# Kernel optimization log

Measured on AMD Instinct MI355X. Metric: run time of the kernel, lower is better.

## Reference

```python
import jax, jax.numpy as jnp
import numpy as np

T = 8192  # context/question length (input_shape[2])
D = 128   # feature dim (input_shape[3])


def setup_inputs() -> dict:
    key = jax.random.key(0)
    k1, k2 = jax.random.split(key)
    x = jax.random.normal(k1, (2, 1, T, D), dtype=jnp.float32)
    kernel = jax.random.normal(k2, (3 * D,), dtype=jnp.float32)
    return {"x": x, "kernel": kernel}


def reference(x, kernel):
    context = x[0, 0]   # (T, D)
    question = x[1, 0]  # (T, D)
    w_c, w_q, w_m = kernel[:D], kernel[D:2 * D], kernel[2 * D:]

    # Additive similarity: S[i,j] = c_i.w_c + q_j.w_q + (c_i*q_j).w_m
    # Avoids materializing the (T, T, 3D) tiled/concatenated tensor.
    S = (context @ w_c)[:, None] + (question @ w_q)[None, :] \
        + (context * w_m) @ question.T  # (T, T)

    A = jax.nn.softmax(S, axis=-1)  # row-wise softmax, as tf.nn.softmax on 2D

    # C2Q attention: U_A[i] = sum_j A[i,j] * q_j
    U_A = A @ question  # (T, D)

    # Q2C attention: b = row-max of A, h = sum_i b_i * c_i, tiled over rows
    b = jnp.max(A, axis=1)          # (T,)
    h = b @ context                 # (D,)
    H_A = jnp.broadcast_to(h, (T, D))

    # megamerge: [c, U_A, c*U_A, c*H_A]
    G = jnp.concatenate([context, U_A, context * U_A, context * H_A], axis=-1)
    return G  # (T, 4D)
```

## Files before the change

kernel.cpp:

```cpp
#include <hip/hip_runtime.h>
#include <hip/hip_bf16.h>

#define T 8192
#define D 128
#define NSPLIT 8
#define JLEN (T / NSPLIT)
#define BN 64
#define NITER (JLEN / BN)
#define BM 128
#define LOG2E 1.44269504088896f

typedef _Float16 half4_t __attribute__((ext_vector_type(4)));
typedef _Float16 half8_t __attribute__((ext_vector_type(8)));
typedef float floatx4 __attribute__((ext_vector_type(4)));

__global__ void prep_kernel(const float* __restrict__ x, const float* __restrict__ kern,
                            _Float16* __restrict__ q16, _Float16* __restrict__ qT16,
                            _Float16* __restrict__ cm16, float* __restrict__ qq2) {
    const float* context  = x;
    const float* question = x + (size_t)T * D;
    const float* wq = kern + D;
    const float* wm = kern + 2 * D;
    __shared__ __align__(16) _Float16 tile[32][136];
    int j0 = blockIdx.x * 32;
    int t = threadIdx.x;
    int c4 = t & 31;
    int rsub = t >> 5;
    float4 wqv = ((const float4*)wq)[c4];
    float4 wmv = ((const float4*)wm)[c4];
    for (int p = 0; p < 4; ++p) {
        int row = p * 8 + rsub;
        float4 q = ((const float4*)(question + (size_t)(j0 + row) * D))[c4];
        float4 c = ((const float4*)(context  + (size_t)(j0 + row) * D))[c4];
        half4_t qh;
        qh[0] = (_Float16)q.x; qh[1] = (_Float16)q.y; qh[2] = (_Float16)q.z; qh[3] = (_Float16)q.w;
        *(half4_t*)(q16 + (size_t)(j0 + row) * D + c4 * 4) = qh;
        *(half4_t*)&tile[row][c4 * 4] = qh;
        half4_t ch;
        ch[0] = (_Float16)(c.x * wmv.x * LOG2E); ch[1] = (_Float16)(c.y * wmv.y * LOG2E);
        ch[2] = (_Float16)(c.z * wmv.z * LOG2E); ch[3] = (_Float16)(c.w * wmv.w * LOG2E);
        *(half4_t*)(cm16 + (size_t)(j0 + row) * D + c4 * 4) = ch;
        float s = q.x * wqv.x + q.y * wqv.y + q.z * wqv.z + q.w * wqv.w;
        for (int dx = 1; dx <= 16; dx <<= 1) s += __shfl_xor(s, dx);
        if (c4 == 0) qq2[j0 + row] = s * LOG2E;
    }
    __syncthreads();
    for (int p = 0; p < 2; ++p) {
        int chunk = t + p * 256;
        int d = chunk >> 2, jo = (chunk & 3) * 8;
        half8_t v;
        for (int s2 = 0; s2 < 8; ++s2) v[s2] = tile[jo + s2][d];
        *(half8_t*)(qT16 + (size_t)d * T + j0 + jo) = v;
    }
}

__global__ __launch_bounds__(256, 2)
void flash_kernel(const _Float16* __restrict__ q16, const _Float16* __restrict__ qT16,
                  const _Float16* __restrict__ cm16, const float* __restrict__ qq2,
                  _Float16* __restrict__ Opart, float* __restrict__ mpart,
                  float* __restrict__ lpart) {
    __shared__ __align__(16) _Float16 Kt[2][64][144];
    __shared__ __align__(16) _Float16 Vt[2][128][72];
    __shared__ __align__(16) float qqs[JLEN];

    int bx = blockIdx.x;
    int rb = bx >> 3;
    int sp = bx & 7;
    int tid = threadIdx.x;
    int wave = tid >> 6;
    int lane = tid & 63;
    int quad = lane >> 4;
    int l15 = lane & 15;
    int rbase = rb * BM + wave * 32;

    ((float4*)qqs)[tid] = ((const float4*)(qq2 + (size_t)sp * JLEN))[tid];

    half8_t qfrag[2][4];
    for (int mt = 0; mt < 2; ++mt)
        for (int ks = 0; ks < 4; ++ks)
            qfrag[mt][ks] = *(const half8_t*)(cm16 + (size_t)(rbase + mt * 16 + l15) * D
                                              + ks * 32 + quad * 8);

    floatx4 acc[2][8];
    for (int mt = 0; mt < 2; ++mt)
        for (int nt = 0; nt < 8; ++nt)
            for (int r = 0; r < 4; ++r) acc[mt][nt][r] = 0.f;
    float m_run[2] = {-INFINITY, -INFINITY};
    float l_run[2] = {0.f, 0.f};

    half8_t kreg[4];
    half4_t vlo[4], vhi[4];

    {
        int j0 = sp * JLEN;
        for (int k = 0; k < 4; ++k) {
            int idx = tid + k * 256;
            kreg[k] = *(const half8_t*)(q16 + (size_t)(j0 + (idx >> 4)) * D + (idx & 15) * 8);
            int dr = idx >> 3, c8 = idx & 7;
            int base = j0 + (c8 >> 2) * 32 + (c8 & 3) * 4;
            vlo[k] = *(const half4_t*)(qT16 + (size_t)dr * T + base);
            vhi[k] = *(const half4_t*)(qT16 + (size_t)dr * T + base + 16);
        }
    }

    for (int it = 0; it < NITER; ++it) {
        int b = it & 1;
        for (int k = 0; k < 4; ++k) {
            int idx = tid + k * 256;
            *(half8_t*)&Kt[b][idx >> 4][(idx & 15) * 8] = kreg[k];
            half8_t v;
            v[0] = vlo[k][0]; v[1] = vlo[k][1]; v[2] = vlo[k][2]; v[3] = vlo[k][3];
            v[4] = vhi[k][0]; v[5] = vhi[k][1]; v[6] = vhi[k][2]; v[7] = vhi[k][3];
            *(half8_t*)&Vt[b][idx >> 3][(idx & 7) * 8] = v;
        }
        __syncthreads();

        if (it + 1 < NITER) {
            int j0n = sp * JLEN + (it + 1) * BN;
            for (int k = 0; k < 4; ++k) {
                int idx = tid + k * 256;
                kreg[k] = *(const half8_t*)(q16 + (size_t)(j0n + (idx >> 4)) * D + (idx & 15) * 8);
                int dr = idx >> 3, c8 = idx & 7;
                int base = j0n + (c8 >> 2) * 32 + (c8 & 3) * 4;
                vlo[k] = *(const half4_t*)(qT16 + (size_t)dr * T + base);
                vhi[k] = *(const half4_t*)(qT16 + (size_t)dr * T + base + 16);
            }
        }

        floatx4 St[2][4];
        for (int mt = 0; mt < 2; ++mt)
            for (int jt = 0; jt < 4; ++jt)
                for (int r = 0; r < 4; ++r) St[mt][jt][r] = 0.f;
        for (int ks = 0; ks < 4; ++ks)
            for (int jt = 0; jt < 4; ++jt) {
                half8_t a = *(const half8_t*)&Kt[b][jt * 16 + l15][ks * 32 + quad * 8];
                St[0][jt] = __builtin_amdgcn_mfma_f32_16x16x32_f16(a, qfrag[0][ks], St[0][jt], 0, 0, 0);
                St[1][jt] = __builtin_amdgcn_mfma_f32_16x16x32_f16(a, qfrag[1][ks], St[1][jt], 0, 0, 0);
            }

        float4 bias[4];
        for (int jt = 0; jt < 4; ++jt)
            bias[jt] = *(const float4*)&qqs[it * 64 + jt * 16 + quad * 4];
        for (int mt = 0; mt < 2; ++mt) {
            St[mt][0][0] += bias[0].x; St[mt][0][1] += bias[0].y; St[mt][0][2] += bias[0].z; St[mt][0][3] += bias[0].w;
            St[mt][1][0] += bias[1].x; St[mt][1][1] += bias[1].y; St[mt][1][2] += bias[1].z; St[mt][1][3] += bias[1].w;
            St[mt][2][0] += bias[2].x; St[mt][2][1] += bias[2].y; St[mt][2][2] += bias[2].z; St[mt][2][3] += bias[2].w;
            St[mt][3][0] += bias[3].x; St[mt][3][1] += bias[3].y; St[mt][3][2] += bias[3].z; St[mt][3][3] += bias[3].w;
        }

        half4_t apv[2][4];
        float alpha[2];
        for (int mt = 0; mt < 2; ++mt) {
            float mx = St[mt][0][0];
            for (int jt = 0; jt < 4; ++jt)
                for (int r = 0; r < 4; ++r) mx = fmaxf(mx, St[mt][jt][r]);
            mx = fmaxf(mx, __shfl_xor(mx, 16));
            mx = fmaxf(mx, __shfl_xor(mx, 32));
            float mnew = fmaxf(m_run[mt], mx);
            alpha[mt] = __builtin_amdgcn_exp2f(m_run[mt] - mnew);
            m_run[mt] = mnew;
            float ps = 0.f;
            for (int jt = 0; jt < 4; ++jt) {
                float p0 = __builtin_amdgcn_exp2f(St[mt][jt][0] - mnew);
                float p1 = __builtin_amdgcn_exp2f(St[mt][jt][1] - mnew);
                float p2 = __builtin_amdgcn_exp2f(St[mt][jt][2] - mnew);
                float p3 = __builtin_amdgcn_exp2f(St[mt][jt][3] - mnew);
                ps += (p0 + p1) + (p2 + p3);
                apv[mt][jt][0] = (_Float16)p0;
                apv[mt][jt][1] = (_Float16)p1;
                apv[mt][jt][2] = (_Float16)p2;
                apv[mt][jt][3] = (_Float16)p3;
            }
            ps += __shfl_xor(ps, 16);
            ps += __shfl_xor(ps, 32);
            l_run[mt] = l_run[mt] * alpha[mt] + ps;
        }
        for (int mt = 0; mt < 2; ++mt) {
            float aT[4];
            for (int r = 0; r < 4; ++r)
                aT[r] = __shfl(alpha[mt], quad * 4 + r);
            for (int nt = 0; nt < 8; ++nt)
                for (int r = 0; r < 4; ++r) acc[mt][nt][r] *= aT[r];
        }

        for (int pr = 0; pr < 2; ++pr) {
            half8_t bb[8];
            for (int nt = 0; nt < 8; ++nt)
                bb[nt] = *(const half8_t*)&Vt[b][nt * 16 + l15][pr * 32 + quad * 8];
            for (int h = 0; h < 2; ++h) {
                int jt = pr * 2 + h;
                for (int nt = 0; nt < 8; ++nt) {
                    half4_t bv;
                    bv[0] = bb[nt][h * 4 + 0]; bv[1] = bb[nt][h * 4 + 1];
                    bv[2] = bb[nt][h * 4 + 2]; bv[3] = bb[nt][h * 4 + 3];
                    acc[0][nt] = __builtin_amdgcn_mfma_f32_16x16x16f16(apv[0][jt], bv, acc[0][nt], 0, 0, 0);
                    acc[1][nt] = __builtin_amdgcn_mfma_f32_16x16x16f16(apv[1][jt], bv, acc[1][nt], 0, 0, 0);
                }
            }
        }
    }

    for (int mt = 0; mt < 2; ++mt) {
        if (quad == 0) {
            int iq = rbase + mt * 16 + l15;
            mpart[(size_t)sp * T + iq] = m_run[mt];
            lpart[(size_t)sp * T + iq] = l_run[mt];
        }
        int i = rbase + mt * 16 + quad * 4;
        for (int nt = 0; nt < 8; ++nt)
            for (int r = 0; r < 4; ++r)
                Opart[((size_t)sp * T + (i + r)) * D + nt * 16 + l15] = (_Float16)acc[mt][nt][r];
    }
}

__global__ void merge_kernel(const _Float16* __restrict__ Opart, const float* __restrict__ mpart,
                             const float* __restrict__ lpart, float* __restrict__ U_A,
                             float* __restrict__ linv) {
    int t = threadIdx.x;
    int i = blockIdx.x * 16 + (t >> 4);
    int c = t & 15;
    float mp[NSPLIT], w[NSPLIT];
    float mstar = -INFINITY;
    for (int sp = 0; sp < NSPLIT; ++sp) {
        mp[sp] = mpart[(size_t)sp * T + i];
        mstar = fmaxf(mstar, mp[sp]);
    }
    float L = 0.f;
    for (int sp = 0; sp < NSPLIT; ++sp) {
        w[sp] = __builtin_amdgcn_exp2f(mp[sp] - mstar);
        L += lpart[(size_t)sp * T + i] * w[sp];
    }
    float invL = 1.0f / L;
    int d0 = c * 8;
    float u[8];
    for (int k = 0; k < 8; ++k) u[k] = 0.f;
    for (int sp = 0; sp < NSPLIT; ++sp) {
        half8_t o = *(const half8_t*)(Opart + ((size_t)sp * T + i) * D + d0);
        for (int k = 0; k < 8; ++k) u[k] += (float)o[k] * w[sp];
    }
    float4 s0 = make_float4(u[0] * invL, u[1] * invL, u[2] * invL, u[3] * invL);
    float4 s1 = make_float4(u[4] * invL, u[5] * invL, u[6] * invL, u[7] * invL);
    *(float4*)(U_A + (size_t)i * D + d0) = s0;
    *(float4*)(U_A + (size_t)i * D + d0 + 4) = s1;
    if (c == 0) linv[i] = invL;
}

__global__ void hsum_part_kernel(const float* __restrict__ x, const float* __restrict__ linv,
                                 float* __restrict__ hpart) {
    const float* context = x;
    int t = threadIdx.x;
    int d = t & 127, g = t >> 7;
    int i0 = blockIdx.x * 128 + g * 64;
    float s = 0.f;
    for (int k = 0; k < 64; ++k)
        s += context[(size_t)(i0 + k) * D + d] * linv[i0 + k];
    hpart[(size_t)(blockIdx.x * 2 + g) * 128 + d] = s;
}

__global__ void hreduce_kernel(const float* __restrict__ hpart, float* __restrict__ h) {
    int d = threadIdx.x;
    float s = 0.f;
    for (int k = 0; k < 128; ++k) s += hpart[(size_t)k * 128 + d];
    h[d] = s;
}

__global__ void assemble_kernel(const float* __restrict__ x, const float* __restrict__ U_A,
                                const float* __restrict__ h, float* __restrict__ out) {
    const float* context = x;
    int gid = blockIdx.x * 256 + threadIdx.x;
    int base = gid * 4;
    int i = base >> 9;
    int c = base & 511;
    int seg = c >> 7, d = c & 127;
    float4 r;
    if (seg == 0) {
        r = *(const float4*)(context + (size_t)i * D + d);
    } else if (seg == 1) {
        r = *(const float4*)(U_A + (size_t)i * D + d);
    } else if (seg == 2) {
        float4 a = *(const float4*)(context + (size_t)i * D + d);
        float4 b = *(const float4*)(U_A + (size_t)i * D + d);
        r = make_float4(a.x * b.x, a.y * b.y, a.z * b.z, a.w * b.w);
    } else {
        float4 a = *(const float4*)(context + (size_t)i * D + d);
        float4 b = *(const float4*)(h + d);
        r = make_float4(a.x * b.x, a.y * b.y, a.z * b.z, a.w * b.w);
    }
    *(float4*)(out + base) = r;
}

extern "C" void kernel_launch(void* const* d_in, const int* in_sizes, int n_in,
                              void* d_out, int out_size, void* d_ws, size_t ws_size,
                              hipStream_t stream) {
    const float* x = (const float*)d_in[0];
    const float* kern = (const float*)d_in[1];
    float* out = (float*)d_out;

    char* w = (char*)d_ws;
    size_t off = 0;
    _Float16* q16  = (_Float16*)(w + off); off += (size_t)T * D * 2;
    _Float16* qT16 = (_Float16*)(w + off); off += (size_t)T * D * 2;
    _Float16* cm16 = (_Float16*)(w + off); off += (size_t)T * D * 2;
    float* qq2   = (float*)(w + off); off += (size_t)T * 4;
    float* mpart = (float*)(w + off); off += (size_t)NSPLIT * T * 4;
    float* lpart = (float*)(w + off); off += (size_t)NSPLIT * T * 4;
    float* U_A   = (float*)(w + off); off += (size_t)T * D * 4;
    float* linv  = (float*)(w + off); off += (size_t)T * 4;
    float* hpart = (float*)(w + off); off += (size_t)128 * 128 * 4;
    float* h     = (float*)(w + off); off += (size_t)D * 4;

    _Float16* Opart = (_Float16*)d_out;

    prep_kernel<<<256, 256, 0, stream>>>(x, kern, q16, qT16, cm16, qq2);
    flash_kernel<<<512, 256, 0, stream>>>(q16, qT16, cm16, qq2, Opart, mpart, lpart);
    merge_kernel<<<512, 256, 0, stream>>>(Opart, mpart, lpart, U_A, linv);
    hsum_part_kernel<<<64, 256, 0, stream>>>(x, linv, hpart);
    hreduce_kernel<<<1, 128, 0, stream>>>(hpart, h);
    assemble_kernel<<<4096, 256, 0, stream>>>(x, U_A, h, out);
}
```

Baseline: 136.2 us.

## Double KV splits, single-buffer LDS, store normalized partial outputs as fp8

Result: slower. 264.2 us (+94.1%).

```diff
diff --git a/kernel.cpp b/kernel.cpp
--- a/kernel.cpp
+++ b/kernel.cpp
@@ -3,7 +3,7 @@
 
 #define T 8192
 #define D 128
-#define NSPLIT 8
+#define NSPLIT 16
 #define JLEN (T / NSPLIT)
 #define BN 64
 #define NITER (JLEN / BN)
@@ -54,18 +54,18 @@
     }
 }
 
-__global__ __launch_bounds__(256, 2)
+__global__ __launch_bounds__(256, 4)
 void flash_kernel(const _Float16* __restrict__ q16, const _Float16* __restrict__ qT16,
                   const _Float16* __restrict__ cm16, const float* __restrict__ qq2,
-                  _Float16* __restrict__ Opart, float* __restrict__ mpart,
+                  unsigned char* __restrict__ Opart, float* __restrict__ mpart,
                   float* __restrict__ lpart) {
-    __shared__ __align__(16) _Float16 Kt[2][64][144];
-    __shared__ __align__(16) _Float16 Vt[2][128][72];
+    __shared__ __align__(16) _Float16 Kt[64][144];
+    __shared__ __align__(16) _Float16 Vt[128][72];
     __shared__ __align__(16) float qqs[JLEN];
 
     int bx = blockIdx.x;
-    int rb = bx >> 3;
-    int sp = bx & 7;
+    int rb = bx >> 4;
+    int sp = bx & 15;
     int tid = threadIdx.x;
     int wave = tid >> 6;
     int lane = tid & 63;
@@ -73,7 +73,8 @@
     int l15 = lane & 15;
     int rbase = rb * BM + wave * 32;
 
-    ((float4*)qqs)[tid] = ((const float4*)(qq2 + (size_t)sp * JLEN))[tid];
+    if (tid < JLEN / 4)
+        ((float4*)qqs)[tid] = ((const float4*)(qq2 + (size_t)sp * JLEN))[tid];
 
     half8_t qfrag[2][4];
     for (int mt = 0; mt < 2; ++mt)
@@ -88,30 +89,24 @@
     float m_run[2] = {-INFINITY, -INFINITY};
     float l_run[2] = {0.f, 0.f};
 
-    half8_t kreg[4];
-    half4_t vlo[4], vhi[4];
-
+    half8_t kreg[4], vreg[4];
     {
         int j0 = sp * JLEN;
         for (int k = 0; k < 4; ++k) {
             int idx = tid + k * 256;
             kreg[k] = *(const half8_t*)(q16 + (size_t)(j0 + (idx >> 4)) * D + (idx & 15) * 8);
-            int dr = idx >> 3, c8 = idx & 7;
-            int base = j0 + (c8 >> 2) * 32 + (c8 & 3) * 4;
-            vlo[k] = *(const half4_t*)(qT16 + (size_t)dr * T + base);
-            vhi[k] = *(const half4_t*)(qT16 + (size_t)dr * T + base + 16);
+            vreg[k] = *(const half8_t*)(qT16 + (size_t)(idx >> 3) * T + j0 + (idx & 7) * 8);
         }
     }
 
     for (int it = 0; it < NITER; ++it) {
-        int b = it & 1;
         for (int k = 0; k < 4; ++k) {
             int idx = tid + k * 256;
-            *(half8_t*)&Kt[b][idx >> 4][(idx & 15) * 8] = kreg[k];
-            half8_t v;
-            v[0] = vlo[k][0]; v[1] = vlo[k][1]; v[2] = vlo[k][2]; v[3] = vlo[k][3];
-            v[4] = vhi[k][0]; v[5] = vhi[k][1]; v[6] = vhi[k][2]; v[7] = vhi[k][3];
-            *(half8_t*)&Vt[b][idx >> 3][(idx & 7) * 8] = v;
+            *(half8_t*)&Kt[idx >> 4][(idx & 15) * 8] = kreg[k];
+        }
+        for (int k = 0; k < 4; ++k) {
+            int idx = tid + k * 256;
+            *(half8_t*)&Vt[idx >> 3][(idx & 7) * 8] = vreg[k];
         }
         __syncthreads();
 
@@ -120,10 +115,7 @@
             for (int k = 0; k < 4; ++k) {
                 int idx = tid + k * 256;
                 kreg[k] = *(const half8_t*)(q16 + (size_t)(j0n + (idx >> 4)) * D + (idx & 15) * 8);
-                int dr = idx >> 3, c8 = idx & 7;
-                int base = j0n + (c8 >> 2) * 32 + (c8 & 3) * 4;
-                vlo[k] = *(const half4_t*)(qT16 + (size_t)dr * T + base);
-                vhi[k] = *(const half4_t*)(qT16 + (size_t)dr * T + base + 16);
+                vreg[k] = *(const half8_t*)(qT16 + (size_t)(idx >> 3) * T + j0n + (idx & 7) * 8);
             }
         }
 
@@ -133,7 +125,7 @@
                 for (int r = 0; r < 4; ++r) St[mt][jt][r] = 0.f;
         for (int ks = 0; ks < 4; ++ks)
             for (int jt = 0; jt < 4; ++jt) {
-                half8_t a = *(const half8_t*)&Kt[b][jt * 16 + l15][ks * 32 + quad * 8];
+                half8_t a = *(const half8_t*)&Kt[jt * 16 + l15][ks * 32 + quad * 8];
                 St[0][jt] = __builtin_amdgcn_mfma_f32_16x16x32_f16(a, qfrag[0][ks], St[0][jt], 0, 0, 0);
                 St[1][jt] = __builtin_amdgcn_mfma_f32_16x16x32_f16(a, qfrag[1][ks], St[1][jt], 0, 0, 0);
             }
@@ -183,21 +175,13 @@
                 for (int r = 0; r < 4; ++r) acc[mt][nt][r] *= aT[r];
         }
 
-        for (int pr = 0; pr < 2; ++pr) {
-            half8_t bb[8];
-            for (int nt = 0; nt < 8; ++nt)
-                bb[nt] = *(const half8_t*)&Vt[b][nt * 16 + l15][pr * 32 + quad * 8];
-            for (int h = 0; h < 2; ++h) {
-                int jt = pr * 2 + h;
-                for (int nt = 0; nt < 8; ++nt) {
-                    half4_t bv;
-                    bv[0] = bb[nt][h * 4 + 0]; bv[1] = bb[nt][h * 4 + 1];
-                    bv[2] = bb[nt][h * 4 + 2]; bv[3] = bb[nt][h * 4 + 3];
-                    acc[0][nt] = __builtin_amdgcn_mfma_f32_16x16x16f16(apv[0][jt], bv, acc[0][nt], 0, 0, 0);
-                    acc[1][nt] = __builtin_amdgcn_mfma_f32_16x16x16f16(apv[1][jt], bv, acc[1][nt], 0, 0, 0);
-                }
-            }
-        }
+        for (int jt = 0; jt < 4; ++jt)
+            for (int nt = 0; nt < 8; ++nt) {
+                half4_t b = *(const half4_t*)&Vt[nt * 16 + l15][jt * 16 + quad * 4];
+                acc[0][nt] = __builtin_amdgcn_mfma_f32_16x16x16f16(apv[0][jt], b, acc[0][nt], 0, 0, 0);
+                acc[1][nt] = __builtin_amdgcn_mfma_f32_16x16x16f16(apv[1][jt], b, acc[1][nt], 0, 0, 0);
+            }
+        __syncthreads();
     }
 
     for (int mt = 0; mt < 2; ++mt) {
@@ -206,38 +190,49 @@
             mpart[(size_t)sp * T + iq] = m_run[mt];
             lpart[(size_t)sp * T + iq] = l_run[mt];
         }
+        float rinv[4];
+        for (int r = 0; r < 4; ++r)
+            rinv[r] = 1.0f / __shfl(l_run[mt], quad * 4 + r);
         int i = rbase + mt * 16 + quad * 4;
         for (int nt = 0; nt < 8; ++nt)
-            for (int r = 0; r < 4; ++r)
-                Opart[((size_t)sp * T + (i + r)) * D + nt * 16 + l15] = (_Float16)acc[mt][nt][r];
-    }
-}
-
-__global__ void merge_kernel(const _Float16* __restrict__ Opart, const float* __restrict__ mpart,
+            for (int r = 0; r < 4; ++r) {
+                float v = acc[mt][nt][r] * rinv[r];
+                int p = __builtin_amdgcn_cvt_pk_fp8_f32(v, v, 0, false);
+                Opart[((size_t)sp * T + (i + r)) * D + nt * 16 + l15] = (unsigned char)(p & 0xFF);
+            }
+    }
+}
+
+__global__ void merge_kernel(const unsigned char* __restrict__ Opart, const float* __restrict__ mpart,
                              const float* __restrict__ lpart, float* __restrict__ U_A,
                              float* __restrict__ linv) {
     int t = threadIdx.x;
     int i = blockIdx.x * 16 + (t >> 4);
     int c = t & 15;
-    float mp[NSPLIT], w[NSPLIT];
+    float mp[NSPLIT];
     float mstar = -INFINITY;
     for (int sp = 0; sp < NSPLIT; ++sp) {
         mp[sp] = mpart[(size_t)sp * T + i];
         mstar = fmaxf(mstar, mp[sp]);
     }
     float L = 0.f;
-    for (int sp = 0; sp < NSPLIT; ++sp) {
-        w[sp] = __builtin_amdgcn_exp2f(mp[sp] - mstar);
-        L += lpart[(size_t)sp * T + i] * w[sp];
-    }
-    float invL = 1.0f / L;
-    int d0 = c * 8;
     float u[8];
     for (int k = 0; k < 8; ++k) u[k] = 0.f;
+    int d0 = c * 8;
     for (int sp = 0; sp < NSPLIT; ++sp) {
-        half8_t o = *(const half8_t*)(Opart + ((size_t)sp * T + i) * D + d0);
-        for (int k = 0; k < 8; ++k) u[k] += (float)o[k] * w[sp];
-    }
+        float w = __builtin_amdgcn_exp2f(mp[sp] - mstar) * lpart[(size_t)sp * T + i];
+        L += w;
+        uint2 ow = *(const uint2*)(Opart + ((size_t)sp * T + i) * D + d0);
+        u[0] += __builtin_amdgcn_cvt_f32_fp8(ow.x, 0) * w;
+        u[1] += __builtin_amdgcn_cvt_f32_fp8(ow.x, 1) * w;
+        u[2] += __builtin_amdgcn_cvt_f32_fp8(ow.x, 2) * w;
+        u[3] += __builtin_amdgcn_cvt_f32_fp8(ow.x, 3) * w;
+        u[4] += __builtin_amdgcn_cvt_f32_fp8(ow.y, 0) * w;
+        u[5] += __builtin_amdgcn_cvt_f32_fp8(ow.y, 1) * w;
+        u[6] += __builtin_amdgcn_cvt_f32_fp8(ow.y, 2) * w;
+        u[7] += __builtin_amdgcn_cvt_f32_fp8(ow.y, 3) * w;
+    }
+    float invL = 1.0f / L;
     float4 s0 = make_float4(u[0] * invL, u[1] * invL, u[2] * invL, u[3] * invL);
     float4 s1 = make_float4(u[4] * invL, u[5] * invL, u[6] * invL, u[7] * invL);
     *(float4*)(U_A + (size_t)i * D + d0) = s0;
@@ -309,10 +304,10 @@
     float* hpart = (float*)(w + off); off += (size_t)128 * 128 * 4;
     float* h     = (float*)(w + off); off += (size_t)D * 4;
 
-    _Float16* Opart = (_Float16*)d_out;
+    unsigned char* Opart = (unsigned char*)d_out;
 
     prep_kernel<<<256, 256, 0, stream>>>(x, kern, q16, qT16, cm16, qq2);
-    flash_kernel<<<512, 256, 0, stream>>>(q16, qT16, cm16, qq2, Opart, mpart, lpart);
+    flash_kernel<<<1024, 256, 0, stream>>>(q16, qT16, cm16, qq2, Opart, mpart, lpart);
     merge_kernel<<<512, 256, 0, stream>>>(Opart, mpart, lpart, U_A, linv);
     hsum_part_kernel<<<64, 256, 0, stream>>>(x, linv, hpart);
     hreduce_kernel<<<1, 128, 0, stream>>>(hpart, h);
```
